# Kernel tuning notes

Measured on AMD Instinct MI355X. Metric: run time of the kernel, lower is better.

Reference implementation:

```python
import jax, jax.numpy as jnp
import numpy as np

EMBED_DIM = 1024
NUM_HEADS = 16
HEAD_DIM = EMBED_DIM // NUM_HEADS
BATCH = 2
SEQ = 2048


def setup_inputs() -> dict:
    key = jax.random.key(0)
    k1, k2, k3, k4, k5 = jax.random.split(key, 5)
    scale_in = 1.0 / np.sqrt(EMBED_DIM)
    return {
        "x": jax.random.normal(k1, (BATCH, SEQ, EMBED_DIM), dtype=jnp.float32),
        "head_mask": jnp.ones((NUM_HEADS,), dtype=jnp.float32),
        "qkv_w": jax.random.normal(k2, (3 * EMBED_DIM, EMBED_DIM), dtype=jnp.float32) * scale_in,
        "qkv_b": jax.random.normal(k3, (3 * EMBED_DIM,), dtype=jnp.float32) * 0.02,
        "fc_w": jax.random.normal(k4, (EMBED_DIM, EMBED_DIM), dtype=jnp.float32) * scale_in,
        "fc_b": jax.random.normal(k5, (EMBED_DIM,), dtype=jnp.float32) * 0.02,
    }


def reference(x, head_mask, qkv_w, qkv_b, fc_w, fc_b):
    N, S, D = x.shape
    H, hd = NUM_HEADS, HEAD_DIM
    # qkv Linear: y = x @ W^T + b -> [N, S, 3D]
    qkv = jnp.einsum("nsd,ed->nse", x, qkv_w) + qkv_b
    # reshape (N, S, H, 3, hd) then permute(3,0,2,1,4) -> (3, N, H, S, hd)
    qkv = qkv.reshape(N, S, H, 3, hd).transpose(3, 0, 2, 1, 4)
    q, k, v = qkv[0], qkv[1], qkv[2]
    hm = head_mask.reshape(1, H, 1, 1)
    q = q * hm
    k = k * hm
    v = v * hm
    # scores [N, H, S, S]
    energy = jnp.einsum("nhqd,nhkd->nhqk", q, k)
    attention = jax.nn.softmax(energy / jnp.sqrt(jnp.float32(hd)), axis=-1)
    out = jnp.einsum("nhqk,nhkd->nhqd", attention, v)
    out = out.transpose(0, 2, 1, 3).reshape(N, S, H * hd)
    out = jnp.einsum("nsd,ed->nse", out, fc_w) + fc_b
    return out
```

## Files before the change

### kernel.cpp

```cpp
#include <hip/hip_runtime.h>
#include <hip/hip_bf16.h>

typedef __bf16 bf16;
typedef __attribute__((ext_vector_type(8))) __bf16 bf16x8;
typedef __attribute__((ext_vector_type(4))) __bf16 bf16x4;
typedef __attribute__((ext_vector_type(4))) float f32x4;
typedef __attribute__((ext_vector_type(4))) unsigned int uint4x;

#if __has_builtin(__builtin_amdgcn_exp2f)
#define EXP2F(x) __builtin_amdgcn_exp2f(x)
#else
#define EXP2F(x) exp2f(x)
#endif

#define AS1 __attribute__((address_space(1)))
#define AS3 __attribute__((address_space(3)))

static __device__ __forceinline__ void async_ld16(const bf16* g, bf16* l) {
  __builtin_amdgcn_global_load_lds((const AS1 void*)g, (AS3 void*)l, 16, 0, 0);
}

static __device__ __forceinline__ unsigned bf16rne(float x) {
  unsigned u = __float_as_uint(x);
  return (u + 0x7fffu + ((u >> 16) & 1u)) >> 16;
}
static __device__ __forceinline__ unsigned pack2(float a, float b) {
  return bf16rne(a) | (bf16rne(b) << 16);
}

__global__ void cvt3_kernel(const float* __restrict__ x, const float* __restrict__ qw,
                            const float* __restrict__ fw, bf16* __restrict__ xb,
                            bf16* __restrict__ qwb, bf16* __restrict__ fwb) {
  int b = blockIdx.x;
  const float* src;
  bf16* dst;
  int i;
  if (b < 4096) { src = x; dst = xb; i = b * 256 + threadIdx.x; }
  else if (b < 7168) { src = qw; dst = qwb; i = (b - 4096) * 256 + threadIdx.x; }
  else { src = fw; dst = fwb; i = (b - 7168) * 256 + threadIdx.x; }
  f32x4 v = *(const f32x4*)(src + (size_t)i * 4);
  bf16x4 o;
  o[0] = (bf16)v[0]; o[1] = (bf16)v[1]; o[2] = (bf16)v[2]; o[3] = (bf16)v[3];
  *(bf16x4*)(dst + (size_t)i * 4) = o;
}

#define GEMM_STAGE(k0_, buf_)                                                    \
  {                                                                              \
    async_ld16(A + (size_t)(rowBase + r0) * Kdim + (k0_) + csw, &As[buf_][f0]);  \
    async_ld16(A + (size_t)(rowBase + r1) * Kdim + (k0_) + csw, &As[buf_][f1]);  \
    async_ld16(Bw + (size_t)(colBase + r0) * Kdim + (k0_) + csw, &Bs[buf_][f0]); \
    async_ld16(Bw + (size_t)(colBase + r1) * Kdim + (k0_) + csw, &Bs[buf_][f1]); \
  }

template <int MODE>
__global__ __launch_bounds__(256, 2) void gemm_bt_kernel(
    const bf16* __restrict__ A, const bf16* __restrict__ Bw,
    const float* __restrict__ bias, const float* __restrict__ hm,
    bf16* __restrict__ Qp, bf16* __restrict__ Kp, bf16* __restrict__ Vp,
    float* __restrict__ outF, int Ncols, int Kdim, int rowBlkCount) {
  __shared__ bf16 As[2][128 * 32];
  __shared__ bf16 Bs[2][128 * 32];
  const int t = threadIdx.x, lane = t & 63, w = t >> 6;
  const int wr = w >> 1, wc = w & 1;
  const int j = lane & 15, quad = lane >> 4;
  const int rowBlk = blockIdx.x % rowBlkCount;
  const int colBlk = blockIdx.x / rowBlkCount;
  const int rowBase = rowBlk * 128, colBase = colBlk * 128;

  f32x4 acc[4][4];
  const f32x4 z4 = {0.f, 0.f, 0.f, 0.f};
#pragma unroll
  for (int i = 0; i < 4; ++i)
#pragma unroll
    for (int jj = 0; jj < 4; ++jj) acc[i][jj] = z4;

  const int f0 = t * 8;
  const int f1 = f0 + 2048;
  const int r0 = f0 >> 5, r1 = r0 + 64;
  const int csw = (((t & 3) ^ ((r0 >> 1) & 3))) * 8;
  const int qsw = (quad ^ ((j >> 1) & 3)) * 8;

  GEMM_STAGE(0, 0);
  if (32 < Kdim) GEMM_STAGE(32, 1);
  int buf = 0;
  for (int k0 = 0; k0 < Kdim; k0 += 32) {
    if (k0 + 32 < Kdim) {
      asm volatile("s_waitcnt vmcnt(4)" ::: "memory");
    } else {
      asm volatile("s_waitcnt vmcnt(0)" ::: "memory");
    }
    __builtin_amdgcn_s_barrier();
    __builtin_amdgcn_sched_barrier(0);
    bf16x8 af[4], bfr[4];
#pragma unroll
    for (int i = 0; i < 4; ++i)
      af[i] = *(const bf16x8*)&As[buf][(wr * 64 + i * 16 + j) * 32 + qsw];
#pragma unroll
    for (int jj = 0; jj < 4; ++jj)
      bfr[jj] = *(const bf16x8*)&Bs[buf][(wc * 64 + jj * 16 + j) * 32 + qsw];
#pragma unroll
    for (int i = 0; i < 4; ++i)
#pragma unroll
      for (int jj = 0; jj < 4; ++jj)
        acc[i][jj] = __builtin_amdgcn_mfma_f32_16x16x32_bf16(af[i], bfr[jj], acc[i][jj], 0, 0, 0);
    __builtin_amdgcn_s_barrier();
    __builtin_amdgcn_sched_barrier(0);
    if (k0 + 64 < Kdim) GEMM_STAGE(k0 + 64, buf);
    buf ^= 1;
  }

  if (MODE == 0) {
#pragma unroll
    for (int jj = 0; jj < 4; ++jj) {
      int col = colBase + wc * 64 + jj * 16 + j;
      int hh = col / 192;
      int rem = col - hh * 192;
      int mm = rem >> 6;
      int dd = rem & 63;
      float hmv = hm[hh];
      float bv = bias[col];
      float sc = (mm == 0) ? hmv * 0.18033688011112042f : hmv;
#pragma unroll
      for (int i = 0; i < 4; ++i) {
#pragma unroll
        for (int r = 0; r < 4; ++r) {
          int row = rowBase + wr * 64 + i * 16 + quad * 4 + r;
          int n = row >> 11, ss = row & 2047;
          size_t nh = (size_t)(n * 16 + hh);
          float val = (acc[i][jj][r] + bv) * sc;
          if (mm == 0) {
            Qp[nh * 131072 + ss * 64 + dd] = (bf16)val;
          } else if (mm == 1) {
            size_t idx = nh * 131072 + (size_t)(ss >> 7) * 8192 +
                         (size_t)(2 * ((ss >> 5) & 3) + ((ss >> 2) & 1)) * 1024 +
                         (dd >> 5) * 512 + ((dd >> 3) & 3) * 128 +
                         (((ss >> 3) & 3) * 4 + (ss & 3)) * 8 + (dd & 7);
            Kp[idx] = (bf16)val;
          } else {
            size_t idx = nh * 131072 + (size_t)(ss >> 7) * 8192 +
                         (((ss >> 5) & 3) * 4 + (dd >> 4)) * 512 +
                         ((ss >> 3) & 3) * 128 + (dd & 15) * 8 + (ss & 7);
            Vp[idx] = (bf16)val;
          }
        }
      }
    }
  } else {
#pragma unroll
    for (int jj = 0; jj < 4; ++jj) {
      int col = colBase + wc * 64 + jj * 16 + j;
      float bv = bias[col];
#pragma unroll
      for (int i = 0; i < 4; ++i)
#pragma unroll
        for (int r = 0; r < 4; ++r) {
          int row = rowBase + wr * 64 + i * 16 + quad * 4 + r;
          outF[(size_t)row * Ncols + col] = acc[i][jj][r] + bv;
        }
    }
  }
}

#define FLASH_STAGE(tileIdx, kOff, vOff)                                    \
  {                                                                         \
    const bf16* kn_ = Kc + (tileIdx) * 2048;                                \
    const bf16* vn_ = Vc + (tileIdx) * 2048;                                \
    int c = ts * 8;                                                         \
    async_ld16(kn_ + c, &KVpool[(kOff) + c]);                               \
    async_ld16(vn_ + c, &KVpool[(vOff) + c]);                               \
  }

#define FLASH_TILE(kOff, vOff)                                              \
  {                                                                         \
    unsigned pkd[2][2][2];                                                  \
    _Pragma("unroll")                                                       \
    for (int ct = 0; ct < 2; ++ct) {                                        \
      bf16x8 kf0 = *(const bf16x8*)&KVpool[(kOff) + ct * 1024 + lane * 8];  \
      bf16x8 kf1 = *(const bf16x8*)&KVpool[(kOff) + ct * 1024 + 512 + lane * 8]; \
      _Pragma("unroll")                                                     \
      for (int rt = 0; rt < 2; ++rt) {                                      \
        f32x4 sv = z4;                                                      \
        __builtin_amdgcn_s_setprio(1);                                      \
        sv = __builtin_amdgcn_mfma_f32_16x16x32_bf16(kf0, qf[rt][0], sv, 0, 0, 0); \
        sv = __builtin_amdgcn_mfma_f32_16x16x32_bf16(kf1, qf[rt][1], sv, 0, 0, 0); \
        __builtin_amdgcn_s_setprio(0);                                      \
        float p0 = EXP2F(sv[0]), p1 = EXP2F(sv[1]);                         \
        float p2 = EXP2F(sv[2]), p3 = EXP2F(sv[3]);                         \
        lrow[rt] += (p0 + p1) + (p2 + p3);                                  \
        pkd[rt][ct][0] = pack2(p0, p1);                                     \
        pkd[rt][ct][1] = pack2(p2, p3);                                     \
      }                                                                     \
    }                                                                       \
    __builtin_amdgcn_s_setprio(1);                                          \
    {                                                                       \
      union { uint4x u; bf16x8 h; } pa[2];                                  \
      _Pragma("unroll")                                                     \
      for (int rt = 0; rt < 2; ++rt)                                        \
        pa[rt].u = (uint4x){pkd[rt][0][0], pkd[rt][0][1],                   \
                            pkd[rt][1][0], pkd[rt][1][1]};                  \
      _Pragma("unroll")                                                     \
      for (int dt = 0; dt < 4; ++dt) {                                      \
        bf16x8 vf = *(const bf16x8*)&KVpool[(vOff) + dt * 512 + lane * 8];  \
        oacc[0][dt] = __builtin_amdgcn_mfma_f32_16x16x32_bf16(pa[0].h, vf, oacc[0][dt], 0, 0, 0); \
        oacc[1][dt] = __builtin_amdgcn_mfma_f32_16x16x32_bf16(pa[1].h, vf, oacc[1][dt], 0, 0, 0); \
      }                                                                     \
    }                                                                       \
    __builtin_amdgcn_s_setprio(0);                                          \
  }

__global__ __launch_bounds__(512, 4) void flash_kernel(const bf16* __restrict__ Qp,
                                                       const bf16* __restrict__ Kf,
                                                       const bf16* __restrict__ Vf,
                                                       bf16* __restrict__ attn) {
  __shared__ bf16 KVpool[16384];
  __shared__ float Lsh[8][32];
  const int t = threadIdx.x, lane = t & 63, w = t >> 6;
  const int ts = t & 255;
  const int hc = t >> 8;
  const int j = lane & 15, quad = lane >> 4;
  const int b = blockIdx.x;
  const int qt = b >> 5;
  const int nh = b & 31;
  const int q0 = qt * 128 + (w & 3) * 32;
  const bf16* Qb = Qp + (size_t)nh * 131072;
  const bf16* Kc = Kf + (size_t)nh * 131072 + hc * 65536;
  const bf16* Vc = Vf + (size_t)nh * 131072 + hc * 65536;

  const int kb0 = (hc * 2 + 0) * 2048, kb1 = (hc * 2 + 1) * 2048;
  const int vb0 = 8192 + kb0, vb1 = 8192 + kb1;

  bf16x8 qf[2][2];
#pragma unroll
  for (int rt = 0; rt < 2; ++rt)
#pragma unroll
    for (int kd = 0; kd < 2; ++kd)
      qf[rt][kd] = *(const bf16x8*)&Qb[(size_t)(q0 + rt * 16 + j) * 64 + kd * 32 + quad * 8];

  float lrow[2] = {0.f, 0.f};
  f32x4 oacc[2][4];
  const f32x4 z4 = {0.f, 0.f, 0.f, 0.f};
#pragma unroll
  for (int rt = 0; rt < 2; ++rt)
#pragma unroll
    for (int dt = 0; dt < 4; ++dt) oacc[rt][dt] = z4;

  FLASH_STAGE(0, kb0, vb0);

  for (int it2 = 0; it2 < 16; ++it2) {
    __syncthreads();
    FLASH_STAGE(it2 * 2 + 1, kb1, vb1);
    FLASH_TILE(kb0, vb0);
    __syncthreads();
    if (it2 < 15) FLASH_STAGE(it2 * 2 + 2, kb0, vb0);
    FLASH_TILE(kb1, vb1);
  }

  float lf[2];
#pragma unroll
  for (int rt = 0; rt < 2; ++rt) {
    float l = lrow[rt];
    l += __shfl_xor(l, 16);
    l += __shfl_xor(l, 32);
    lf[rt] = l;
  }
  __syncthreads();
  if (quad == 0) {
    Lsh[w][j] = lf[0];
    Lsh[w][16 + j] = lf[1];
  }
  float* Osh = (float*)&KVpool[0];
  if (w >= 4) {
    int wb = w - 4;
#pragma unroll
    for (int rt = 0; rt < 2; ++rt)
#pragma unroll
      for (int dt = 0; dt < 4; ++dt)
#pragma unroll
        for (int r = 0; r < 4; ++r)
          Osh[((((wb * 2 + rt) * 4 + dt) * 4) + r) * 64 + lane] = oacc[rt][dt][r];
  }
  __syncthreads();
  if (w < 4) {
    int n = nh >> 4, h = nh & 15;
    float inv[2][4];
#pragma unroll
    for (int rt = 0; rt < 2; ++rt)
#pragma unroll
      for (int r = 0; r < 4; ++r) {
        int idx = rt * 16 + quad * 4 + r;
        inv[rt][r] = 1.0f / (Lsh[w][idx] + Lsh[w + 4][idx]);
      }
#pragma unroll
    for (int rt = 0; rt < 2; ++rt)
#pragma unroll
      for (int r = 0; r < 4; ++r) {
        int s = q0 + rt * 16 + quad * 4 + r;
        size_t base = ((size_t)(n * 2048 + s)) * 1024 + h * 64;
#pragma unroll
        for (int dt = 0; dt < 4; ++dt) {
          float o = oacc[rt][dt][r] +
                    Osh[((((w * 2 + rt) * 4 + dt) * 4) + r) * 64 + lane];
          attn[base + dt * 16 + j] = (bf16)(o * inv[rt][r]);
        }
      }
  }
}

extern "C" void kernel_launch(void* const* d_in, const int* in_sizes, int n_in,
                              void* d_out, int out_size, void* d_ws, size_t ws_size,
                              hipStream_t stream) {
  const float* x = (const float*)d_in[0];
  const float* head_mask = (const float*)d_in[1];
  const float* qkv_w = (const float*)d_in[2];
  const float* qkv_b = (const float*)d_in[3];
  const float* fc_w = (const float*)d_in[4];
  const float* fc_b = (const float*)d_in[5];
  float* out = (float*)d_out;

  char* ws = (char*)d_ws;
  bf16* x_bf    = (bf16*)(ws + 0);
  bf16* qkvw_bf = (bf16*)(ws + ((size_t)8 << 20));
  bf16* fcw_bf  = (bf16*)(ws + ((size_t)14 << 20));
  bf16* Qp      = (bf16*)(ws + ((size_t)16 << 20));
  bf16* Kf      = (bf16*)(ws + ((size_t)24 << 20));
  bf16* Vf      = (bf16*)(ws + ((size_t)32 << 20));
  bf16* attn = x_bf;

  cvt3_kernel<<<8192, 256, 0, stream>>>(x, qkv_w, fc_w, x_bf, qkvw_bf, fcw_bf);
  gemm_bt_kernel<0><<<32 * 24, 256, 0, stream>>>(x_bf, qkvw_bf, qkv_b, head_mask,
                                                 Qp, Kf, Vf, nullptr, 3072, 1024, 32);
  flash_kernel<<<512, 512, 0, stream>>>(Qp, Kf, Vf, attn);
  gemm_bt_kernel<1><<<32 * 8, 256, 0, stream>>>(attn, fcw_bf, fc_b, nullptr,
                                                nullptr, nullptr, nullptr, out, 1024, 1024, 32);
}
```

Measured before the change: 185.2 us.

## Load K/V fragments directly from global into registers, dropping LDS staging

```diff
diff --git a/kernel.cpp b/kernel.cpp
--- a/kernel.cpp
+++ b/kernel.cpp
@@ -161,28 +161,33 @@
   }
 }
 
-#define FLASH_STAGE(tileIdx, kOff, vOff)                                    \
+#define FLASH_LOADK(tt, KF)                                                 \
   {                                                                         \
-    const bf16* kn_ = Kc + (tileIdx) * 2048;                                \
-    const bf16* vn_ = Vc + (tileIdx) * 2048;                                \
-    int c = ts * 8;                                                         \
-    async_ld16(kn_ + c, &KVpool[(kOff) + c]);                               \
-    async_ld16(vn_ + c, &KVpool[(vOff) + c]);                               \
-  }
-
-#define FLASH_TILE(kOff, vOff)                                              \
+    _Pragma("unroll")                                                       \
+    for (int c_ = 0; c_ < 2; ++c_) {                                        \
+      (KF)[c_][0] = *(const bf16x8*)&Kc[(tt) * 2048 + c_ * 1024 + lane * 8];\
+      (KF)[c_][1] = *(const bf16x8*)&Kc[(tt) * 2048 + c_ * 1024 + 512 + lane * 8]; \
+    }                                                                       \
+  }
+
+#define FLASH_LOADV(tt, VV)                                                 \
+  {                                                                         \
+    _Pragma("unroll")                                                       \
+    for (int d_ = 0; d_ < 4; ++d_)                                          \
+      (VV)[d_] = *(const bf16x8*)&Vc[(tt) * 2048 + d_ * 512 + lane * 8];    \
+  }
+
+#define FLASH_TILE(KF, VV)                                                  \
   {                                                                         \
     unsigned pkd[2][2][2];                                                  \
     _Pragma("unroll")                                                       \
     for (int ct = 0; ct < 2; ++ct) {                                        \
-      bf16x8 kf0 = *(const bf16x8*)&KVpool[(kOff) + ct * 1024 + lane * 8];  \
-      bf16x8 kf1 = *(const bf16x8*)&KVpool[(kOff) + ct * 1024 + 512 + lane * 8]; \
       _Pragma("unroll")                                                     \
       for (int rt = 0; rt < 2; ++rt) {                                      \
         f32x4 sv = z4;                                                      \
         __builtin_amdgcn_s_setprio(1);                                      \
-        sv = __builtin_amdgcn_mfma_f32_16x16x32_bf16(kf0, qf[rt][0], sv, 0, 0, 0); \
-        sv = __builtin_amdgcn_mfma_f32_16x16x32_bf16(kf1, qf[rt][1], sv, 0, 0, 0); \
+        sv = __builtin_amdgcn_mfma_f32_16x16x32_bf16((KF)[ct][0], qf[rt][0], sv, 0, 0, 0); \
+        sv = __builtin_amdgcn_mfma_f32_16x16x32_bf16((KF)[ct][1], qf[rt][1], sv, 0, 0, 0); \
         __builtin_amdgcn_s_setprio(0);                                      \
         float p0 = EXP2F(sv[0]), p1 = EXP2F(sv[1]);                         \
         float p2 = EXP2F(sv[2]), p3 = EXP2F(sv[3]);                         \
@@ -200,9 +205,8 @@
                             pkd[rt][1][0], pkd[rt][1][1]};                  \
       _Pragma("unroll")                                                     \
       for (int dt = 0; dt < 4; ++dt) {                                      \
-        bf16x8 vf = *(const bf16x8*)&KVpool[(vOff) + dt * 512 + lane * 8];  \
-        oacc[0][dt] = __builtin_amdgcn_mfma_f32_16x16x32_bf16(pa[0].h, vf, oacc[0][dt], 0, 0, 0); \
-        oacc[1][dt] = __builtin_amdgcn_mfma_f32_16x16x32_bf16(pa[1].h, vf, oacc[1][dt], 0, 0, 0); \
+        oacc[0][dt] = __builtin_amdgcn_mfma_f32_16x16x32_bf16(pa[0].h, (VV)[dt], oacc[0][dt], 0, 0, 0); \
+        oacc[1][dt] = __builtin_amdgcn_mfma_f32_16x16x32_bf16(pa[1].h, (VV)[dt], oacc[1][dt], 0, 0, 0); \
       }                                                                     \
     }                                                                       \
     __builtin_amdgcn_s_setprio(0);                                          \
@@ -215,8 +219,7 @@
   __shared__ bf16 KVpool[16384];
   __shared__ float Lsh[8][32];
   const int t = threadIdx.x, lane = t & 63, w = t >> 6;
-  const int ts = t & 255;
-  const int hc = t >> 8;
+  const int hc = w >> 2;
   const int j = lane & 15, quad = lane >> 4;
   const int b = blockIdx.x;
   const int qt = b >> 5;
@@ -226,9 +229,6 @@
   const bf16* Kc = Kf + (size_t)nh * 131072 + hc * 65536;
   const bf16* Vc = Vf + (size_t)nh * 131072 + hc * 65536;
 
-  const int kb0 = (hc * 2 + 0) * 2048, kb1 = (hc * 2 + 1) * 2048;
-  const int vb0 = 8192 + kb0, vb1 = 8192 + kb1;
-
   bf16x8 qf[2][2];
 #pragma unroll
   for (int rt = 0; rt < 2; ++rt)
@@ -244,15 +244,18 @@
 #pragma unroll
     for (int dt = 0; dt < 4; ++dt) oacc[rt][dt] = z4;
 
-  FLASH_STAGE(0, kb0, vb0);
-
-  for (int it2 = 0; it2 < 16; ++it2) {
-    __syncthreads();
-    FLASH_STAGE(it2 * 2 + 1, kb1, vb1);
-    FLASH_TILE(kb0, vb0);
-    __syncthreads();
-    if (it2 < 15) FLASH_STAGE(it2 * 2 + 2, kb0, vb0);
-    FLASH_TILE(kb1, vb1);
+  bf16x8 kA[2][2], kB[2][2], vv[4];
+  FLASH_LOADK(0, kA);
+  FLASH_LOADV(0, vv);
+
+  for (int st2 = 0; st2 < 16; ++st2) {
+    const int t0 = st2 * 2, t1 = t0 + 1;
+    FLASH_LOADK(t1, kB);
+    FLASH_TILE(kA, vv);
+    FLASH_LOADV(t1, vv);
+    if (st2 < 15) FLASH_LOADK(t1 + 1, kA);
+    FLASH_TILE(kB, vv);
+    if (st2 < 15) FLASH_LOADV(t1 + 1, vv);
   }
 
   float lf[2];
```

New measurement: 185.2 us. About the same (+0.0%).
